# Kernel optimization log

Hardware: AMD Instinct MI355X
Metric: run time of the kernel (lower is better)

## Reference

```python
import jax, jax.numpy as jnp
import numpy as np

SPARSITY = 0.9  # target fraction of zeros (magnitude pruning)
D_IN = 4096
D_OUT = 4096
TOKENS = 4096


def setup_inputs() -> dict:
    key = jax.random.key(0)
    k1, k2 = jax.random.split(key)
    x = jax.random.normal(k1, (TOKENS, D_IN), dtype=jnp.float32)
    weight = jax.random.normal(k2, (D_OUT, D_IN), dtype=jnp.float32) * 0.01
    bias = jnp.zeros((D_OUT,), dtype=jnp.float32)
    return {"x": x, "weight": weight, "bias": bias}


def reference(x, weight, bias):
    # Magnitude pruning: threshold at the SPARSITY quantile of |W|,
    # keep only entries strictly above threshold (matches CSR build),
    # then sparse-dense GEMM y = x @ W_pruned^T + b.
    aw = jnp.abs(weight)
    thr = jnp.quantile(aw, SPARSITY)
    w_pruned = jnp.where(aw > thr, weight, jnp.zeros_like(weight))
    return x @ w_pruned.T + bias
```

## Files before the change

### kernel.cpp

```cpp
#include <hip/hip_runtime.h>
#include <stdint.h>

#define D_IN   4096
#define D_OUT  4096
#define NTOK   4096
#define NW     (D_OUT * D_IN)
#define RANK1  15099493u
#define CAP    1500000

typedef unsigned int  uint32;
typedef unsigned short ushort_t;
typedef float  f32x4  __attribute__((ext_vector_type(4)));
typedef __bf16 bf16x8 __attribute__((ext_vector_type(8)));

__device__ __forceinline__ uint32 rne_bf16(float f) {
  uint32 u = __float_as_uint(f);
  return (u + 0x7FFFu + ((u >> 16) & 1u)) >> 16;
}

__device__ __forceinline__ void gload_lds16(const void* g, void* l) {
  __builtin_amdgcn_global_load_lds((__attribute__((address_space(1))) void*)(g),
                                   (__attribute__((address_space(3))) void*)(l), 16, 0, 0);
}

template <int NB>
__device__ __forceinline__ void dsel(const uint32* __restrict__ h, uint32 rank,
                                     uint32* res, uint32* wtot) {
  constexpr int PER = NB >> 8;
  int tid = threadIdx.x;
  int lane = tid & 63, wid = tid >> 6;
  uint32 loc[PER];
  uint32 s = 0;
  int base = tid * PER;
#pragma unroll
  for (int i = 0; i < PER; i++) { loc[i] = h[base + i]; s += loc[i]; }
  uint32 v = s;
  for (int d = 1; d < 64; d <<= 1) { uint32 o = __shfl_up(v, (unsigned)d); if (lane >= d) v += o; }
  if (lane == 63) wtot[wid] = v;
  __syncthreads();
  uint32 woff = 0;
  for (int w = 0; w < wid; w++) woff += wtot[w];
  uint32 incl = v + woff, excl = incl - s;
  if (rank >= excl && rank < incl) {
    uint32 c = excl;
#pragma unroll
    for (int i = 0; i < PER; i++) {
      if (rank < c + loc[i]) { res[0] = (uint32)(base + i); res[1] = rank - c; break; }
      c += loc[i];
    }
  }
  __syncthreads();
}

__global__ void k1_hist1_convx(const uint4* __restrict__ wb, uint32* __restrict__ hist,
                               const float4* __restrict__ x, uint4* __restrict__ xout) {
  __shared__ uint32 lh[4][2048];
  if (blockIdx.x < 2048) {
    for (int i = threadIdx.x; i < 8192; i += 256) ((uint32*)lh)[i] = 0;
    __syncthreads();
    int wid = threadIdx.x >> 6;
    int idx = blockIdx.x * 256 + threadIdx.x;
    for (int i = idx; i < NW / 4; i += 2048 * 256) {
      uint4 v = wb[i];
      atomicAdd(&lh[wid][(v.x & 0x7FFFFFFFu) >> 20], 1u);
      atomicAdd(&lh[wid][(v.y & 0x7FFFFFFFu) >> 20], 1u);
      atomicAdd(&lh[wid][(v.z & 0x7FFFFFFFu) >> 20], 1u);
      atomicAdd(&lh[wid][(v.w & 0x7FFFFFFFu) >> 20], 1u);
    }
    __syncthreads();
    for (int i = threadIdx.x; i < 2048; i += 256) {
      uint32 c = lh[0][i] + lh[1][i] + lh[2][i] + lh[3][i];
      if (c) atomicAdd(&hist[i], c);
    }
  } else {
    int i = (blockIdx.x - 2048) * 256 + threadIdx.x;
    for (; i < NW / 8; i += 3072 * 256) {
      float4 a = x[2 * i], b = x[2 * i + 1];
      uint4 o;
      o.x = rne_bf16(a.x) | (rne_bf16(a.y) << 16);
      o.y = rne_bf16(a.z) | (rne_bf16(a.w) << 16);
      o.z = rne_bf16(b.x) | (rne_bf16(b.y) << 16);
      o.w = rne_bf16(b.z) | (rne_bf16(b.w) << 16);
      xout[i] = o;
    }
  }
}

__global__ void k2_decide(const float4* __restrict__ w, const uint32* __restrict__ hist1,
                          uint4* __restrict__ out, uint2* __restrict__ cand,
                          uint32* __restrict__ cnt, uint32* __restrict__ hs1) {
  __shared__ uint32 res1[2], wt[4];
  __shared__ uint32 lcnt, lbase;
  __shared__ uint2 lbuf[3072];
  __shared__ uint32 lch[1024];
  for (int i = threadIdx.x; i < 1024; i += 256) lch[i] = 0;
  if (threadIdx.x == 0) lcnt = 0;
  dsel<2048>(hist1, RANK1, res1, wt);
  uint32 bstar = res1[0];
  int i = blockIdx.x * 256 + threadIdx.x;
  for (; i < NW / 8; i += 2048 * 256) {
    float4 a = w[2 * i], b = w[2 * i + 1];
    float f[8] = {a.x, a.y, a.z, a.w, b.x, b.y, b.z, b.w};
    uint32 h[8];
#pragma unroll
    for (int j = 0; j < 8; j++) {
      uint32 bits = __float_as_uint(f[j]);
      uint32 bin = (bits & 0x7FFFFFFFu) >> 20;
      h[j] = (bin > bstar) ? rne_bf16(f[j]) : 0u;
      if (bin == bstar) {
        uint32 p = atomicAdd(&lcnt, 1u);
        if (p < 3072) {
          lbuf[p] = make_uint2((uint32)(8 * i + j), bits);
          atomicAdd(&lch[(bits >> 10) & 1023u], 1u);
        }
      }
    }
    uint4 o;
    o.x = h[0] | (h[1] << 16);
    o.y = h[2] | (h[3] << 16);
    o.z = h[4] | (h[5] << 16);
    o.w = h[6] | (h[7] << 16);
    out[i] = o;
  }
  __syncthreads();
  uint32 nstore = lcnt < 3072u ? lcnt : 3072u;
  if (threadIdx.x == 0) lbase = atomicAdd(cnt, nstore);
  __syncthreads();
  for (uint32 p = threadIdx.x; p < nstore; p += 256) {
    uint32 g = lbase + p;
    if (g < CAP) cand[g] = lbuf[p];
  }
  for (int ii = threadIdx.x; ii < 1024; ii += 256) if (lch[ii]) atomicAdd(&hs1[ii], lch[ii]);
}

__global__ void s2_hist(const uint2* __restrict__ cand, const uint32* __restrict__ cnt,
                        const uint32* __restrict__ hist1, const uint32* __restrict__ hs1,
                        uint32* __restrict__ hs2) {
  __shared__ uint32 lh[1024];
  __shared__ uint32 res1[2], res2[2], wt[4];
  for (int i = threadIdx.x; i < 1024; i += 256) lh[i] = 0;
  dsel<2048>(hist1, RANK1, res1, wt);
  dsel<1024>(hs1, res1[1], res2, wt);
  uint32 b2 = res2[0];
  uint32 n = *cnt; if (n > CAP) n = CAP;
  for (uint32 i = blockIdx.x * 256 + threadIdx.x; i < n; i += gridDim.x * 256) {
    uint32 mag = cand[i].y & 0x7FFFFFFFu;
    if (((mag >> 10) & 1023u) == b2) atomicAdd(&lh[mag & 1023u], 1u);
  }
  __syncthreads();
  for (int i = threadIdx.x; i < 1024; i += 256) if (lh[i]) atomicAdd(&hs2[i], lh[i]);
}

__global__ void k5_fixup(const uint2* __restrict__ cand, const uint32* __restrict__ cnt,
                         const uint32* __restrict__ hist1, const uint32* __restrict__ hs1,
                         const uint32* __restrict__ hs2, ushort_t* __restrict__ wb) {
  __shared__ uint32 res1[2], res2[2], res3[2], wt[4];
  dsel<2048>(hist1, RANK1, res1, wt);
  dsel<1024>(hs1, res1[1], res2, wt);
  dsel<1024>(hs2, res2[1], res3, wt);
  uint32 thr_mag = (res1[0] << 20) | (res2[0] << 10) | res3[0];
  uint32 n = *cnt; if (n > CAP) n = CAP;
  for (uint32 i = blockIdx.x * 256 + threadIdx.x; i < n; i += gridDim.x * 256) {
    uint2 c = cand[i];
    uint32 mag = c.y & 0x7FFFFFFFu;
    if (mag > thr_mag) wb[c.x] = (ushort_t)rne_bf16(__uint_as_float(c.y));
  }
}

#define TILES 128

#define MF16(AF, BF, MO)                                                                          \
  acc[(MO)+0][0] = __builtin_amdgcn_mfma_f32_16x16x32_bf16(AF[0], BF[0], acc[(MO)+0][0], 0,0,0);  \
  acc[(MO)+0][1] = __builtin_amdgcn_mfma_f32_16x16x32_bf16(AF[0], BF[1], acc[(MO)+0][1], 0,0,0);  \
  acc[(MO)+0][2] = __builtin_amdgcn_mfma_f32_16x16x32_bf16(AF[0], BF[2], acc[(MO)+0][2], 0,0,0);  \
  acc[(MO)+0][3] = __builtin_amdgcn_mfma_f32_16x16x32_bf16(AF[0], BF[3], acc[(MO)+0][3], 0,0,0);  \
  acc[(MO)+1][0] = __builtin_amdgcn_mfma_f32_16x16x32_bf16(AF[1], BF[0], acc[(MO)+1][0], 0,0,0);  \
  acc[(MO)+1][1] = __builtin_amdgcn_mfma_f32_16x16x32_bf16(AF[1], BF[1], acc[(MO)+1][1], 0,0,0);  \
  acc[(MO)+1][2] = __builtin_amdgcn_mfma_f32_16x16x32_bf16(AF[1], BF[2], acc[(MO)+1][2], 0,0,0);  \
  acc[(MO)+1][3] = __builtin_amdgcn_mfma_f32_16x16x32_bf16(AF[1], BF[3], acc[(MO)+1][3], 0,0,0);  \
  acc[(MO)+2][0] = __builtin_amdgcn_mfma_f32_16x16x32_bf16(AF[2], BF[0], acc[(MO)+2][0], 0,0,0);  \
  acc[(MO)+2][1] = __builtin_amdgcn_mfma_f32_16x16x32_bf16(AF[2], BF[1], acc[(MO)+2][1], 0,0,0);  \
  acc[(MO)+2][2] = __builtin_amdgcn_mfma_f32_16x16x32_bf16(AF[2], BF[2], acc[(MO)+2][2], 0,0,0);  \
  acc[(MO)+2][3] = __builtin_amdgcn_mfma_f32_16x16x32_bf16(AF[2], BF[3], acc[(MO)+2][3], 0,0,0);  \
  acc[(MO)+3][0] = __builtin_amdgcn_mfma_f32_16x16x32_bf16(AF[3], BF[0], acc[(MO)+3][0], 0,0,0);  \
  acc[(MO)+3][1] = __builtin_amdgcn_mfma_f32_16x16x32_bf16(AF[3], BF[1], acc[(MO)+3][1], 0,0,0);  \
  acc[(MO)+3][2] = __builtin_amdgcn_mfma_f32_16x16x32_bf16(AF[3], BF[2], acc[(MO)+3][2], 0,0,0);  \
  acc[(MO)+3][3] = __builtin_amdgcn_mfma_f32_16x16x32_bf16(AF[3], BF[3], acc[(MO)+3][3], 0,0,0);

#define GBODY(T, S, SN)                                                        \
  {                                                                            \
    const bf16x8* A8n = (const bf16x8*)(lds + (((T) + 1) & 3) * 16384);        \
    const bf16x8* B8n = A8n + 1024;                                            \
    bv[SN][0]  = B8n[(br +  0) * 4 + csel];                                    \
    bv[SN][1]  = B8n[(br + 16) * 4 + csel];                                    \
    bv[SN][2]  = B8n[(br + 32) * 4 + csel];                                    \
    bv[SN][3]  = B8n[(br + 48) * 4 + csel];                                    \
    a03[SN][0] = A8n[(ar +  0) * 4 + csel];                                    \
    a03[SN][1] = A8n[(ar + 16) * 4 + csel];                                    \
    a03[SN][2] = A8n[(ar + 32) * 4 + csel];                                    \
    a03[SN][3] = A8n[(ar + 48) * 4 + csel];                                    \
    __builtin_amdgcn_sched_barrier(0);                                         \
    ushort_t* sb = lds + (((T) + 3) & 3) * 16384;                              \
    gload_lds16(pA0, sb + ld0);                                                \
    gload_lds16(pA1, sb + ld1);                                                \
    gload_lds16(pB0, sb + 8192 + ld0);                                         \
    gload_lds16(pB1, sb + 8192 + ld1);                                         \
    __builtin_amdgcn_sched_barrier(0);                                         \
    asm volatile("s_waitcnt lgkmcnt(8)" ::: "memory");                         \
    __builtin_amdgcn_sched_barrier(0);                                         \
    __builtin_amdgcn_s_setprio(1);                                             \
    MF16(a47[S], bv[S], 4)                                                     \
    __builtin_amdgcn_s_setprio(0);                                             \
    __builtin_amdgcn_sched_barrier(0);                                         \
    a47[SN][0] = A8n[(ar +  64) * 4 + csel];                                   \
    a47[SN][1] = A8n[(ar +  80) * 4 + csel];                                   \
    a47[SN][2] = A8n[(ar +  96) * 4 + csel];                                   \
    a47[SN][3] = A8n[(ar + 112) * 4 + csel];                                   \
    __builtin_amdgcn_sched_barrier(0);                                         \
    asm volatile("s_waitcnt lgkmcnt(4)" ::: "memory");                         \
    asm volatile("s_waitcnt vmcnt(4)" ::: "memory");                           \
    asm volatile("s_barrier" ::: "memory");                                    \
    __builtin_amdgcn_sched_barrier(0);                                         \
    __builtin_amdgcn_s_setprio(1);                                             \
    MF16(a03[SN], bv[SN], 0)                                                   \
    __builtin_amdgcn_s_setprio(0);                                             \
    __builtin_amdgcn_sched_barrier(0);                                         \
    if ((T) < TILES - 4) { pA0 += 32; pA1 += 32; pB0 += 32; pB1 += 32; }       \
  }

__global__ __launch_bounds__(512, 2) void gemm_bt(const ushort_t* __restrict__ A,
                                                  const ushort_t* __restrict__ B,
                                                  const float* __restrict__ bias,
                                                  float* __restrict__ C) {
  extern __shared__ ushort_t lds[];

  int bid = blockIdx.x;
  int swz = (bid & 7) * 32 + (bid >> 3);
  int bm = swz >> 4;
  int bn = swz & 15;

  int tid  = threadIdx.x;
  int lane = tid & 63;
  int wave = tid >> 6;
  int wm = wave >> 2, wn = wave & 3;

  int l15  = lane & 15;
  int csel = (lane >> 4) ^ ((lane >> 1) & 3);

  int idx0 = tid, idx1 = 512 + tid;
  int sr0 = idx0 >> 2, scl0 = (idx0 & 3) ^ ((sr0 >> 1) & 3);
  int sr1 = idx1 >> 2, scl1 = (idx1 & 3) ^ ((sr1 >> 1) & 3);
  int ld0 = idx0 * 8, ld1 = idx1 * 8;
  const ushort_t* pA0 = A + (size_t)(bm * 256 + sr0) * D_IN + scl0 * 8;
  const ushort_t* pA1 = A + (size_t)(bm * 256 + sr1) * D_IN + scl1 * 8;
  const ushort_t* pB0 = B + (size_t)(bn * 256 + sr0) * D_IN + scl0 * 8;
  const ushort_t* pB1 = B + (size_t)(bn * 256 + sr1) * D_IN + scl1 * 8;

  f32x4 acc[8][4];
#pragma unroll
  for (int m = 0; m < 8; m++)
#pragma unroll
    for (int n = 0; n < 4; n++) acc[m][n] = (f32x4){0.f, 0.f, 0.f, 0.f};

  gload_lds16(pA0,      lds + ld0);         gload_lds16(pA1,      lds + ld1);
  gload_lds16(pB0,      lds + 8192 + ld0);  gload_lds16(pB1,      lds + 8192 + ld1);
  gload_lds16(pA0 + 32, lds + 16384 + ld0); gload_lds16(pA1 + 32, lds + 16384 + ld1);
  gload_lds16(pB0 + 32, lds + 24576 + ld0); gload_lds16(pB1 + 32, lds + 24576 + ld1);
  gload_lds16(pA0 + 64, lds + 32768 + ld0); gload_lds16(pA1 + 64, lds + 32768 + ld1);
  gload_lds16(pB0 + 64, lds + 40960 + ld0); gload_lds16(pB1 + 64, lds + 40960 + ld1);
  pA0 += 96; pA1 += 96; pB0 += 96; pB1 += 96;
  asm volatile("s_waitcnt vmcnt(4)" ::: "memory");
  asm volatile("s_barrier" ::: "memory");

  int ar = wm * 128 + l15;
  int br = wn * 64 + l15;

  bf16x8 bv[2][4], a03[2][4], a47[2][4];

  {
    const bf16x8* A8 = (const bf16x8*)lds;
    const bf16x8* B8 = A8 + 1024;
    bv[0][0]  = B8[(br +  0) * 4 + csel];
    bv[0][1]  = B8[(br + 16) * 4 + csel];
    bv[0][2]  = B8[(br + 32) * 4 + csel];
    bv[0][3]  = B8[(br + 48) * 4 + csel];
    a03[0][0] = A8[(ar +  0) * 4 + csel];
    a03[0][1] = A8[(ar + 16) * 4 + csel];
    a03[0][2] = A8[(ar + 32) * 4 + csel];
    a03[0][3] = A8[(ar + 48) * 4 + csel];
    __builtin_amdgcn_sched_barrier(0);
    a47[0][0] = A8[(ar +  64) * 4 + csel];
    a47[0][1] = A8[(ar +  80) * 4 + csel];
    a47[0][2] = A8[(ar +  96) * 4 + csel];
    a47[0][3] = A8[(ar + 112) * 4 + csel];
    __builtin_amdgcn_sched_barrier(0);
    asm volatile("s_waitcnt lgkmcnt(4)" ::: "memory");
    __builtin_amdgcn_sched_barrier(0);
    __builtin_amdgcn_s_setprio(1);
    MF16(a03[0], bv[0], 0)
    __builtin_amdgcn_s_setprio(0);
    __builtin_amdgcn_sched_barrier(0);
  }

  for (int tt = 0; tt < 63; tt++) {
    int t0 = tt * 2;
    GBODY(t0, 0, 1)
    GBODY(t0 + 1, 1, 0)
  }
  GBODY(126, 0, 1)

  asm volatile("s_waitcnt lgkmcnt(0)" ::: "memory");
  __builtin_amdgcn_sched_barrier(0);
  __builtin_amdgcn_s_setprio(1);
  MF16(a47[1], bv[1], 4)
  __builtin_amdgcn_s_setprio(0);

  int orow0 = bm * 256 + wm * 128 + (lane >> 4) * 4;
  int ocol0 = bn * 256 + wn * 64 + l15;
#pragma unroll
  for (int n = 0; n < 4; n++) {
    float bb = bias[ocol0 + n * 16];
#pragma unroll
    for (int m = 0; m < 8; m++) {
#pragma unroll
      for (int r = 0; r < 4; r++) {
        C[(size_t)(orow0 + m * 16 + r) * D_OUT + ocol0 + n * 16] = acc[m][n][r] + bb;
      }
    }
  }
}

extern "C" void kernel_launch(void* const* d_in, const int* in_sizes, int n_in,
                              void* d_out, int out_size, void* d_ws, size_t ws_size,
                              hipStream_t stream) {
  const float* x = (const float*)d_in[0];
  const float* w = (const float*)d_in[1];
  const float* bias = (const float*)d_in[2];
  float* out = (float*)d_out;

  char* ws = (char*)d_ws;
  uint32* hist1 = (uint32*)ws;
  uint32* hs1   = (uint32*)(ws + 8192);
  uint32* hs2   = (uint32*)(ws + 12288);
  uint32* cnt   = (uint32*)(ws + 16384);
  ushort_t* Xb  = (ushort_t*)(ws + 65536);
  ushort_t* Wb  = (ushort_t*)(ws + 65536 + (size_t)NW * 2);
  uint2*   cand = (uint2*)(ws + 65536 + (size_t)NW * 4);

  hipMemsetAsync(d_ws, 0, 16448, stream);

  k1_hist1_convx<<<5120, 256, 0, stream>>>((const uint4*)w, hist1, (const float4*)x, (uint4*)Xb);
  k2_decide<<<2048, 256, 0, stream>>>((const float4*)w, hist1, (uint4*)Wb, cand, cnt, hs1);
  s2_hist<<<128, 256, 0, stream>>>(cand, cnt, hist1, hs1, hs2);
  k5_fixup<<<256, 256, 0, stream>>>(cand, cnt, hist1, hs1, hs2, Wb);

  gemm_bt<<<256, 512, 131072, stream>>>(Xb, Wb, bias, out);
}
```

Measured before the change: 232.4 us.

## Switch GEMM to 32x32x16 MFMA tiles and shrink preprocessing grids

Replaces the 16x16x32 bf16 MFMA inner loop with 32x32x16 MFMAs, which changes the fragment layout, the LDS read pattern (two k-halves per tile), the accumulator shape and the output write mapping. Larger MFMAs need fewer LDS fragment reads per FLOP and fewer instructions issued. Separately, it reduces the grid sizes of the histogram/convert and decide kernels so each block loops more times. The risks are higher register pressure from 16-wide accumulators, possible LDS bank conflicts under the new swizzle, and lower occupancy in the preprocessing kernels.

```diff
diff --git a/kernel.cpp b/kernel.cpp
--- a/kernel.cpp
+++ b/kernel.cpp
@@ -10,7 +10,7 @@
 
 typedef unsigned int  uint32;
 typedef unsigned short ushort_t;
-typedef float  f32x4  __attribute__((ext_vector_type(4)));
+typedef float  f32x16 __attribute__((ext_vector_type(16)));
 typedef __bf16 bf16x8 __attribute__((ext_vector_type(8)));
 
 __device__ __forceinline__ uint32 rne_bf16(float f) {
@@ -74,7 +74,7 @@
     }
   } else {
     int i = (blockIdx.x - 2048) * 256 + threadIdx.x;
-    for (; i < NW / 8; i += 3072 * 256) {
+    for (; i < NW / 8; i += 1024 * 256) {
       float4 a = x[2 * i], b = x[2 * i + 1];
       uint4 o;
       o.x = rne_bf16(a.x) | (rne_bf16(a.y) << 16);
@@ -98,7 +98,7 @@
   dsel<2048>(hist1, RANK1, res1, wt);
   uint32 bstar = res1[0];
   int i = blockIdx.x * 256 + threadIdx.x;
-  for (; i < NW / 8; i += 2048 * 256) {
+  for (; i < NW / 8; i += 512 * 256) {
     float4 a = w[2 * i], b = w[2 * i + 1];
     float f[8] = {a.x, a.y, a.z, a.w, b.x, b.y, b.z, b.w};
     uint32 h[8];
@@ -169,36 +169,30 @@
 
 #define TILES 128
 
-#define MF16(AF, BF, MO)                                                                          \
-  acc[(MO)+0][0] = __builtin_amdgcn_mfma_f32_16x16x32_bf16(AF[0], BF[0], acc[(MO)+0][0], 0,0,0);  \
-  acc[(MO)+0][1] = __builtin_amdgcn_mfma_f32_16x16x32_bf16(AF[0], BF[1], acc[(MO)+0][1], 0,0,0);  \
-  acc[(MO)+0][2] = __builtin_amdgcn_mfma_f32_16x16x32_bf16(AF[0], BF[2], acc[(MO)+0][2], 0,0,0);  \
-  acc[(MO)+0][3] = __builtin_amdgcn_mfma_f32_16x16x32_bf16(AF[0], BF[3], acc[(MO)+0][3], 0,0,0);  \
-  acc[(MO)+1][0] = __builtin_amdgcn_mfma_f32_16x16x32_bf16(AF[1], BF[0], acc[(MO)+1][0], 0,0,0);  \
-  acc[(MO)+1][1] = __builtin_amdgcn_mfma_f32_16x16x32_bf16(AF[1], BF[1], acc[(MO)+1][1], 0,0,0);  \
-  acc[(MO)+1][2] = __builtin_amdgcn_mfma_f32_16x16x32_bf16(AF[1], BF[2], acc[(MO)+1][2], 0,0,0);  \
-  acc[(MO)+1][3] = __builtin_amdgcn_mfma_f32_16x16x32_bf16(AF[1], BF[3], acc[(MO)+1][3], 0,0,0);  \
-  acc[(MO)+2][0] = __builtin_amdgcn_mfma_f32_16x16x32_bf16(AF[2], BF[0], acc[(MO)+2][0], 0,0,0);  \
-  acc[(MO)+2][1] = __builtin_amdgcn_mfma_f32_16x16x32_bf16(AF[2], BF[1], acc[(MO)+2][1], 0,0,0);  \
-  acc[(MO)+2][2] = __builtin_amdgcn_mfma_f32_16x16x32_bf16(AF[2], BF[2], acc[(MO)+2][2], 0,0,0);  \
-  acc[(MO)+2][3] = __builtin_amdgcn_mfma_f32_16x16x32_bf16(AF[2], BF[3], acc[(MO)+2][3], 0,0,0);  \
-  acc[(MO)+3][0] = __builtin_amdgcn_mfma_f32_16x16x32_bf16(AF[3], BF[0], acc[(MO)+3][0], 0,0,0);  \
-  acc[(MO)+3][1] = __builtin_amdgcn_mfma_f32_16x16x32_bf16(AF[3], BF[1], acc[(MO)+3][1], 0,0,0);  \
-  acc[(MO)+3][2] = __builtin_amdgcn_mfma_f32_16x16x32_bf16(AF[3], BF[2], acc[(MO)+3][2], 0,0,0);  \
-  acc[(MO)+3][3] = __builtin_amdgcn_mfma_f32_16x16x32_bf16(AF[3], BF[3], acc[(MO)+3][3], 0,0,0);
+#define MFMA32(A, B, ACC) __builtin_amdgcn_mfma_f32_32x32x16_bf16(A, B, ACC, 0, 0, 0)
+
+#define MF8(AF, B0, B1)                    \
+  acc[0] = MFMA32(AF[0], B0, acc[0]);      \
+  acc[1] = MFMA32(AF[0], B1, acc[1]);      \
+  acc[2] = MFMA32(AF[1], B0, acc[2]);      \
+  acc[3] = MFMA32(AF[1], B1, acc[3]);      \
+  acc[4] = MFMA32(AF[2], B0, acc[4]);      \
+  acc[5] = MFMA32(AF[2], B1, acc[5]);      \
+  acc[6] = MFMA32(AF[3], B0, acc[6]);      \
+  acc[7] = MFMA32(AF[3], B1, acc[7]);
 
 #define GBODY(T, S, SN)                                                        \
   {                                                                            \
     const bf16x8* A8n = (const bf16x8*)(lds + (((T) + 1) & 3) * 16384);        \
     const bf16x8* B8n = A8n + 1024;                                            \
-    bv[SN][0]  = B8n[(br +  0) * 4 + csel];                                    \
-    bv[SN][1]  = B8n[(br + 16) * 4 + csel];                                    \
-    bv[SN][2]  = B8n[(br + 32) * 4 + csel];                                    \
-    bv[SN][3]  = B8n[(br + 48) * 4 + csel];                                    \
-    a03[SN][0] = A8n[(ar +  0) * 4 + csel];                                    \
-    a03[SN][1] = A8n[(ar + 16) * 4 + csel];                                    \
-    a03[SN][2] = A8n[(ar + 32) * 4 + csel];                                    \
-    a03[SN][3] = A8n[(ar + 48) * 4 + csel];                                    \
+    bv[SN][0]   = B8n[(br +  0) * 4 + cs0];                                    \
+    bv[SN][1]   = B8n[(br +  0) * 4 + cs1];                                    \
+    bv[SN][2]   = B8n[(br + 32) * 4 + cs0];                                    \
+    bv[SN][3]   = B8n[(br + 32) * 4 + cs1];                                    \
+    afs0[SN][0] = A8n[(ar +  0) * 4 + cs0];                                    \
+    afs0[SN][1] = A8n[(ar + 32) * 4 + cs0];                                    \
+    afs0[SN][2] = A8n[(ar + 64) * 4 + cs0];                                    \
+    afs0[SN][3] = A8n[(ar + 96) * 4 + cs0];                                    \
     __builtin_amdgcn_sched_barrier(0);                                         \
     ushort_t* sb = lds + (((T) + 3) & 3) * 16384;                              \
     gload_lds16(pA0, sb + ld0);                                                \
@@ -209,20 +203,20 @@
     asm volatile("s_waitcnt lgkmcnt(8)" ::: "memory");                         \
     __builtin_amdgcn_sched_barrier(0);                                         \
     __builtin_amdgcn_s_setprio(1);                                             \
-    MF16(a47[S], bv[S], 4)                                                     \
+    MF8(afs1[S], bv[S][1], bv[S][3])                                           \
     __builtin_amdgcn_s_setprio(0);                                             \
     __builtin_amdgcn_sched_barrier(0);                                         \
-    a47[SN][0] = A8n[(ar +  64) * 4 + csel];                                   \
-    a47[SN][1] = A8n[(ar +  80) * 4 + csel];                                   \
-    a47[SN][2] = A8n[(ar +  96) * 4 + csel];                                   \
-    a47[SN][3] = A8n[(ar + 112) * 4 + csel];                                   \
+    afs1[SN][0] = A8n[(ar +  0) * 4 + cs1];                                    \
+    afs1[SN][1] = A8n[(ar + 32) * 4 + cs1];                                    \
+    afs1[SN][2] = A8n[(ar + 64) * 4 + cs1];                                    \
+    afs1[SN][3] = A8n[(ar + 96) * 4 + cs1];                                    \
     __builtin_amdgcn_sched_barrier(0);                                         \
     asm volatile("s_waitcnt lgkmcnt(4)" ::: "memory");                         \
     asm volatile("s_waitcnt vmcnt(4)" ::: "memory");                           \
     asm volatile("s_barrier" ::: "memory");                                    \
     __builtin_amdgcn_sched_barrier(0);                                         \
     __builtin_amdgcn_s_setprio(1);                                             \
-    MF16(a03[SN], bv[SN], 0)                                                   \
+    MF8(afs0[SN], bv[SN][0], bv[SN][2])                                        \
     __builtin_amdgcn_s_setprio(0);                                             \
     __builtin_amdgcn_sched_barrier(0);                                         \
     if ((T) < TILES - 4) { pA0 += 32; pA1 += 32; pB0 += 32; pB1 += 32; }       \
@@ -244,8 +238,11 @@
   int wave = tid >> 6;
   int wm = wave >> 2, wn = wave & 3;
 
-  int l15  = lane & 15;
-  int csel = (lane >> 4) ^ ((lane >> 1) & 3);
+  int l31  = lane & 31;
+  int xr   = (lane >> 1) & 3;
+  int kc   = lane >> 5;
+  int cs0  = kc ^ xr;
+  int cs1  = cs0 ^ 2;
 
   int idx0 = tid, idx1 = 512 + tid;
   int sr0 = idx0 >> 2, scl0 = (idx0 & 3) ^ ((sr0 >> 1) & 3);
@@ -256,11 +253,11 @@
   const ushort_t* pB0 = B + (size_t)(bn * 256 + sr0) * D_IN + scl0 * 8;
   const ushort_t* pB1 = B + (size_t)(bn * 256 + sr1) * D_IN + scl1 * 8;
 
-  f32x4 acc[8][4];
+  f32x16 acc[8];
 #pragma unroll
   for (int m = 0; m < 8; m++)
 #pragma unroll
-    for (int n = 0; n < 4; n++) acc[m][n] = (f32x4){0.f, 0.f, 0.f, 0.f};
+    for (int r = 0; r < 16; r++) acc[m][r] = 0.f;
 
   gload_lds16(pA0,      lds + ld0);         gload_lds16(pA1,      lds + ld1);
   gload_lds16(pB0,      lds + 8192 + ld0);  gload_lds16(pB1,      lds + 8192 + ld1);
@@ -272,32 +269,32 @@
   asm volatile("s_waitcnt vmcnt(4)" ::: "memory");
   asm volatile("s_barrier" ::: "memory");
 
-  int ar = wm * 128 + l15;
-  int br = wn * 64 + l15;
-
-  bf16x8 bv[2][4], a03[2][4], a47[2][4];
+  int ar = wm * 128 + l31;
+  int br = wn * 64 + l31;
+
+  bf16x8 bv[2][4], afs0[2][4], afs1[2][4];
 
   {
     const bf16x8* A8 = (const bf16x8*)lds;
     const bf16x8* B8 = A8 + 1024;
-    bv[0][0]  = B8[(br +  0) * 4 + csel];
-    bv[0][1]  = B8[(br + 16) * 4 + csel];
-    bv[0][2]  = B8[(br + 32) * 4 + csel];
-    bv[0][3]  = B8[(br + 48) * 4 + csel];
-    a03[0][0] = A8[(ar +  0) * 4 + csel];
-    a03[0][1] = A8[(ar + 16) * 4 + csel];
-    a03[0][2] = A8[(ar + 32) * 4 + csel];
-    a03[0][3] = A8[(ar + 48) * 4 + csel];
+    bv[0][0]   = B8[(br +  0) * 4 + cs0];
+    bv[0][1]   = B8[(br +  0) * 4 + cs1];
+    bv[0][2]   = B8[(br + 32) * 4 + cs0];
+    bv[0][3]   = B8[(br + 32) * 4 + cs1];
+    afs0[0][0] = A8[(ar +  0) * 4 + cs0];
+    afs0[0][1] = A8[(ar + 32) * 4 + cs0];
+    afs0[0][2] = A8[(ar + 64) * 4 + cs0];
+    afs0[0][3] = A8[(ar + 96) * 4 + cs0];
     __builtin_amdgcn_sched_barrier(0);
-    a47[0][0] = A8[(ar +  64) * 4 + csel];
-    a47[0][1] = A8[(ar +  80) * 4 + csel];
-    a47[0][2] = A8[(ar +  96) * 4 + csel];
-    a47[0][3] = A8[(ar + 112) * 4 + csel];
+    afs1[0][0] = A8[(ar +  0) * 4 + cs1];
+    afs1[0][1] = A8[(ar + 32) * 4 + cs1];
+    afs1[0][2] = A8[(ar + 64) * 4 + cs1];
+    afs1[0][3] = A8[(ar + 96) * 4 + cs1];
     __builtin_amdgcn_sched_barrier(0);
     asm volatile("s_waitcnt lgkmcnt(4)" ::: "memory");
     __builtin_amdgcn_sched_barrier(0);
     __builtin_amdgcn_s_setprio(1);
-    MF16(a03[0], bv[0], 0)
+    MF8(afs0[0], bv[0][0], bv[0][2])
     __builtin_amdgcn_s_setprio(0);
     __builtin_amdgcn_sched_barrier(0);
   }
@@ -312,19 +309,20 @@
   asm volatile("s_waitcnt lgkmcnt(0)" ::: "memory");
   __builtin_amdgcn_sched_barrier(0);
   __builtin_amdgcn_s_setprio(1);
-  MF16(a47[1], bv[1], 4)
+  MF8(afs1[1], bv[1][1], bv[1][3])
   __builtin_amdgcn_s_setprio(0);
 
-  int orow0 = bm * 256 + wm * 128 + (lane >> 4) * 4;
-  int ocol0 = bn * 256 + wn * 64 + l15;
-#pragma unroll
-  for (int n = 0; n < 4; n++) {
-    float bb = bias[ocol0 + n * 16];
-#pragma unroll
-    for (int m = 0; m < 8; m++) {
-#pragma unroll
-      for (int r = 0; r < 4; r++) {
-        C[(size_t)(orow0 + m * 16 + r) * D_OUT + ocol0 + n * 16] = acc[m][n][r] + bb;
+  int orow0 = bm * 256 + wm * 128 + 4 * (lane >> 5);
+  int ocol0 = bn * 256 + wn * 64 + l31;
+#pragma unroll
+  for (int ni = 0; ni < 2; ni++) {
+    float bb = bias[ocol0 + ni * 32];
+#pragma unroll
+    for (int mi = 0; mi < 4; mi++) {
+#pragma unroll
+      for (int r = 0; r < 16; r++) {
+        int row = orow0 + mi * 32 + (r & 3) + 8 * (r >> 2);
+        C[(size_t)row * D_OUT + ocol0 + ni * 32] = acc[mi * 2 + ni][r] + bb;
       }
     }
   }
@@ -349,8 +347,8 @@
 
   hipMemsetAsync(d_ws, 0, 16448, stream);
 
-  k1_hist1_convx<<<5120, 256, 0, stream>>>((const uint4*)w, hist1, (const float4*)x, (uint4*)Xb);
-  k2_decide<<<2048, 256, 0, stream>>>((const float4*)w, hist1, (uint4*)Wb, cand, cnt, hs1);
+  k1_hist1_convx<<<3072, 256, 0, stream>>>((const uint4*)w, hist1, (const float4*)x, (uint4*)Xb);
+  k2_decide<<<512, 256, 0, stream>>>((const float4*)w, hist1, (uint4*)Wb, cand, cnt, hs1);
   s2_hist<<<128, 256, 0, stream>>>(cand, cnt, hist1, hs1, hs2);
   k5_fixup<<<256, 256, 0, stream>>>(cand, cnt, hist1, hs1, hs2, Wb);
 
```

Result: faster. 222.2 us (-4.4%).
